# Kernel optimization log

Measured on AMD Instinct MI355X. Metric: run time of the kernel, lower is better.

The kernel has to match this reference:

```python
import jax, jax.numpy as jnp
import numpy as np

D_MODEL = 768
NUM_HEADS = 12
D_K = D_MODEL // NUM_HEADS
D_FF = 2048
LN_EPS = 1e-3  # Keras LayerNormalization default
B, S = 4, 2048


def layer_norm(x, gamma, beta):
    mu = jnp.mean(x, axis=-1, keepdims=True)
    var = jnp.var(x, axis=-1, keepdims=True)
    return (x - mu) * jax.lax.rsqrt(var + LN_EPS) * gamma + beta


def setup_inputs() -> dict:
    key = jax.random.key(0)
    ks = jax.random.split(key, 16)
    sd = 0.02
    inp = {
        "x": jax.random.normal(ks[0], (B, S, D_MODEL), dtype=jnp.float32),
        "src_mask": jnp.zeros((B, 1, 1, S), dtype=jnp.float32),
        "Wq": jax.random.normal(ks[1], (D_MODEL, D_MODEL), jnp.float32) * sd,
        "bq": jnp.zeros((D_MODEL,), jnp.float32),
        "Wk": jax.random.normal(ks[2], (D_MODEL, D_MODEL), jnp.float32) * sd,
        "bk": jnp.zeros((D_MODEL,), jnp.float32),
        "Wv": jax.random.normal(ks[3], (D_MODEL, D_MODEL), jnp.float32) * sd,
        "bv": jnp.zeros((D_MODEL,), jnp.float32),
        "Wo": jax.random.normal(ks[4], (D_MODEL, D_MODEL), jnp.float32) * sd,
        "bo": jnp.zeros((D_MODEL,), jnp.float32),
        "W1": jax.random.normal(ks[5], (D_MODEL, D_FF), jnp.float32) * sd,
        "b1": jnp.zeros((D_FF,), jnp.float32),
        "W2": jax.random.normal(ks[6], (D_FF, D_MODEL), jnp.float32) * sd,
        "b2": jnp.zeros((D_MODEL,), jnp.float32),
        "gamma1": jnp.ones((D_MODEL,), jnp.float32),
        "beta1": jnp.zeros((D_MODEL,), jnp.float32),
        "gamma2": jnp.ones((D_MODEL,), jnp.float32),
        "beta2": jnp.zeros((D_MODEL,), jnp.float32),
    }
    return inp


def encoder_layer(x, src_mask, Wq, bq, Wk, bk, Wv, bv, Wo, bo, W1, b1, W2, b2,
                  gamma1, beta1, gamma2, beta2):
    b, s, _ = x.shape
    def heads(t):  # [B,S,D] -> [B,H,S,Dk]
        return t.reshape(b, s, NUM_HEADS, D_K).transpose(0, 2, 1, 3)
    Q = heads(x @ Wq + bq)
    K = heads(x @ Wk + bk)
    V = heads(x @ Wv + bv)
    scores = jnp.einsum("bhqd,bhkd->bhqk", Q, K) / jnp.sqrt(jnp.float32(D_K))
    scores = scores + src_mask * (-1e9)
    probs = jax.nn.softmax(scores, axis=-1)
    attn = jnp.einsum("bhqk,bhkd->bhqd", probs, V)
    attn = attn.transpose(0, 2, 1, 3).reshape(b, s, D_MODEL)
    attn_out = attn @ Wo + bo
    # dropout is identity at inference
    x1 = layer_norm(x + attn_out, gamma1, beta1)
    ff = jax.nn.relu(x1 @ W1 + b1) @ W2 + b2
    return layer_norm(x1 + ff, gamma2, beta2)


def reference(x, src_mask, Wq, bq, Wk, bk, Wv, bv, Wo, bo, W1, b1, W2, b2,
              gamma1, beta1, gamma2, beta2):
    return encoder_layer(x, src_mask, Wq, bq, Wk, bk, Wv, bv, Wo, bo,
                         W1, b1, W2, b2, gamma1, beta1, gamma2, beta2)
```

## Files before the change

kernel.cpp:

```cpp
#include <hip/hip_runtime.h>


typedef unsigned short u16;
typedef __bf16 bf16x8 __attribute__((ext_vector_type(8)));
typedef __bf16 bf16x4 __attribute__((ext_vector_type(4)));
typedef unsigned short u16x8 __attribute__((ext_vector_type(8)));
typedef float f32x4 __attribute__((ext_vector_type(4)));

#define D_MODEL 768
#define D_FF    2048
#define NH      12
#define DK      64
#define S_LEN   2048
#define M_TOK   8192

#define QSCALE   0.18033688011112042f
#define MSCALE  -1.4426950408889634e9f

__device__ __forceinline__ float bf2f(u16 v) {
    union { unsigned u; float f; } c; c.u = ((unsigned)v) << 16; return c.f;
}
__device__ __forceinline__ void st_bf(u16* p, float v) { *(__bf16*)p = (__bf16)v; }

__device__ __forceinline__ void gload_lds16(const void* g, void* l) {
    __builtin_amdgcn_global_load_lds(
        (const __attribute__((address_space(1))) void*)g,
        (__attribute__((address_space(3))) void*)l, 16, 0, 0);
}

__global__ __launch_bounds__(256)
void prep_k(const float* __restrict__ x, const float* __restrict__ Wq,
            const float* __restrict__ Wk, const float* __restrict__ Wv,
            const float* __restrict__ Wo, const float* __restrict__ W1,
            const float* __restrict__ W2, u16* __restrict__ xb,
            u16* __restrict__ WqkvT, u16* __restrict__ WoT,
            u16* __restrict__ W1T, u16* __restrict__ W2T) {
    __shared__ float t[32][33];
    const int id = blockIdx.x, tid = threadIdx.x;
    if (id >= 5376) {
        const int i = ((id - 5376) * 256 + tid) * 4;
        const float4 v = *(const float4*)(x + i);
        __bf16 o[4] = {(__bf16)v.x, (__bf16)v.y, (__bf16)v.z, (__bf16)v.w};
        *(bf16x4*)(xb + i) = *(bf16x4*)o;
        return;
    }
    const float* in; u16* out; int R, C, bx, by;
    if (id < 2304) {
        const int z = id / 576, r = id % 576;
        in = z == 0 ? Wq : (z == 1 ? Wk : (z == 2 ? Wv : Wo));
        out = z == 3 ? WoT : WqkvT + z * 768 * 768;
        R = 768; C = 768; bx = (r % 24) * 32; by = (r / 24) * 32;
    } else if (id < 3840) {
        const int r = id - 2304;
        in = W1; out = W1T; R = 768; C = 2048;
        bx = (r % 64) * 32; by = (r / 64) * 32;
    } else {
        const int r = id - 3840;
        in = W2; out = W2T; R = 2048; C = 768;
        bx = (r % 24) * 32; by = (r / 24) * 32;
    }
    const int tx = tid & 31, ty = tid >> 5;
#pragma unroll
    for (int i = 0; i < 32; i += 8)
        t[ty + i][tx] = in[(size_t)(by + ty + i) * C + bx + tx];
    __syncthreads();
#pragma unroll
    for (int i = 0; i < 32; i += 8)
        st_bf(&out[(size_t)(bx + ty + i) * R + by + tx], t[tx][ty + i]);
}

__global__ __launch_bounds__(256, 3)
void qkv_gemm_k(const u16* __restrict__ A, const u16* __restrict__ Bt,
                const float* __restrict__ bq, const float* __restrict__ bk,
                const float* __restrict__ bv, u16* __restrict__ Qb,
                u16* __restrict__ Kb, u16* __restrict__ Vt) {
    __shared__ __align__(16) u16 As[2][128 * 32];
    __shared__ __align__(16) u16 Bs[2][128 * 32];
    const int tid = threadIdx.x;
    const int lane = tid & 63, w = tid >> 6;
    const int r16 = lane & 15, qd = lane >> 4;
    const int qdx = (qd ^ ((r16 >> 1) & 3)) << 3;
    const int m0 = blockIdx.x * 128, n0 = blockIdx.y * 128;
    const int wm = (w & 1) << 6, wn = (w >> 1) << 6;
    const int K = D_MODEL;

    f32x4 acc[4][4] = {};

    const u16* aP[2]; const u16* bP[2]; int f8[2];
#pragma unroll
    for (int it = 0; it < 2; ++it) {
        const int f = it * 256 + tid;
        const int row = f >> 2;
        const int kc = ((f & 3) ^ ((f >> 3) & 3)) << 3;
        aP[it] = A  + (size_t)(m0 + row) * K + kc;
        bP[it] = Bt + (size_t)(n0 + row) * K + kc;
        f8[it] = f * 8;
    }

    for (int k0 = 0; k0 < K; k0 += 64) {
#pragma unroll
        for (int p = 0; p < 2; ++p)
#pragma unroll
            for (int it = 0; it < 2; ++it) {
                gload_lds16(aP[it] + k0 + p * 32, &As[p][f8[it]]);
                gload_lds16(bP[it] + k0 + p * 32, &Bs[p][f8[it]]);
            }
        __syncthreads();
#pragma unroll
        for (int p = 0; p < 2; ++p) {
            bf16x8 af[4], bfr[4];
#pragma unroll
            for (int i = 0; i < 4; ++i) {
                af[i]  = *(const bf16x8*)&As[p][(wm + i * 16 + r16) * 32 + qdx];
                bfr[i] = *(const bf16x8*)&Bs[p][(wn + i * 16 + r16) * 32 + qdx];
            }
#pragma unroll
            for (int i = 0; i < 4; ++i)
#pragma unroll
                for (int j = 0; j < 4; ++j)
                    acc[i][j] = __builtin_amdgcn_mfma_f32_16x16x32_bf16(af[i], bfr[j], acc[i][j], 0, 0, 0);
        }
        __syncthreads();
    }

    const int sel = n0 < 768 ? 0 : (n0 < 1536 ? 1 : 2);
    const float* bias = sel == 0 ? bq : (sel == 1 ? bk : bv);
    const float scale = sel == 0 ? QSCALE : 1.0f;
    const int nbase = n0 - sel * 768;

#pragma unroll
    for (int j = 0; j < 4; ++j) {
        const int ncol = nbase + wn + j * 16 + r16;
        const float bvv = bias[ncol];
#pragma unroll
        for (int i = 0; i < 4; ++i) {
            if (sel == 2) {
                const int h = ncol >> 6, d = ncol & 63;
                const int mb = m0 + wm + i * 16 + qd * 4;
                const int bb = mb >> 11, npb = mb & 2047;
                __bf16 pk[4];
#pragma unroll
                for (int rr = 0; rr < 4; ++rr) pk[rr] = (__bf16)(acc[i][j][rr] + bvv);
                *(bf16x4*)&Vt[(((size_t)(bb * NH + h)) * DK + d) * S_LEN + npb] = *(bf16x4*)pk;
            } else {
#pragma unroll
                for (int rr = 0; rr < 4; ++rr) {
                    const int m = m0 + wm + i * 16 + qd * 4 + rr;
                    const float v = (acc[i][j][rr] + bvv) * scale;
                    if (sel == 0) st_bf(&Qb[(size_t)m * D_MODEL + ncol], v);
                    else          st_bf(&Kb[(size_t)m * D_MODEL + ncol], v);
                }
            }
        }
    }
}

__global__ __launch_bounds__(256, 3)
void gemm_bt64_k(const u16* __restrict__ A, const u16* __restrict__ Bt,
                 const float* __restrict__ bias, u16* __restrict__ Cout,
                 int M, int N, int K, int mode) {
    __shared__ __align__(16) u16 As[2][64 * 32];
    __shared__ __align__(16) u16 Bs[2][128 * 32];
    const int tid = threadIdx.x;
    const int lane = tid & 63, w = tid >> 6;
    const int r16 = lane & 15, qd = lane >> 4;
    const int qdx = (qd ^ ((r16 >> 1) & 3)) << 3;
    const int m0 = blockIdx.x * 64, n0 = blockIdx.y * 128;
    const int wm = (w & 1) << 5, wn = (w >> 1) << 6;

    f32x4 acc[2][4] = {};

    const int arow = tid >> 2;
    const int akc = (((tid & 3) ^ ((tid >> 3) & 3)) << 3);
    const u16* aP = A + (size_t)(m0 + arow) * K + akc;
    const u16* bP[2]; int f8[2];
#pragma unroll
    for (int it = 0; it < 2; ++it) {
        const int f = it * 256 + tid;
        const int row = f >> 2;
        const int kc = ((f & 3) ^ ((f >> 3) & 3)) << 3;
        bP[it] = Bt + (size_t)(n0 + row) * K + kc;
        f8[it] = f * 8;
    }

    for (int k0 = 0; k0 < K; k0 += 64) {
#pragma unroll
        for (int p = 0; p < 2; ++p) {
            gload_lds16(aP + k0 + p * 32, &As[p][tid * 8]);
#pragma unroll
            for (int it = 0; it < 2; ++it)
                gload_lds16(bP[it] + k0 + p * 32, &Bs[p][f8[it]]);
        }
        __syncthreads();
#pragma unroll
        for (int p = 0; p < 2; ++p) {
            bf16x8 af[2], bfr[4];
#pragma unroll
            for (int i = 0; i < 2; ++i)
                af[i] = *(const bf16x8*)&As[p][(wm + i * 16 + r16) * 32 + qdx];
#pragma unroll
            for (int j = 0; j < 4; ++j)
                bfr[j] = *(const bf16x8*)&Bs[p][(wn + j * 16 + r16) * 32 + qdx];
#pragma unroll
            for (int i = 0; i < 2; ++i)
#pragma unroll
                for (int j = 0; j < 4; ++j)
                    acc[i][j] = __builtin_amdgcn_mfma_f32_16x16x32_bf16(af[i], bfr[j], acc[i][j], 0, 0, 0);
        }
        __syncthreads();
    }

#pragma unroll
    for (int j = 0; j < 4; ++j) {
        const int n = n0 + wn + j * 16 + r16;
        const float bv = bias ? bias[n] : 0.0f;
#pragma unroll
        for (int i = 0; i < 2; ++i) {
#pragma unroll
            for (int rr = 0; rr < 4; ++rr) {
                const int m = m0 + wm + i * 16 + qd * 4 + rr;
                float v = acc[i][j][rr] + bv;
                if (mode == 2) v = fmaxf(v, 0.0f);
                st_bf(&Cout[(size_t)m * N + n], v);
            }
        }
    }
}

__global__ __launch_bounds__(512, 2)
void ff1_k(const u16* __restrict__ A, const u16* __restrict__ Bt,
           const float* __restrict__ bias, u16* __restrict__ C) {
    __shared__ __align__(16) u16 AB[2][32768];
    const int tid = threadIdx.x, lane = tid & 63;
    const int w = tid >> 6;
    const int wm2 = w >> 2, wn4 = w & 3;
    const int r16 = lane & 15, qd = lane >> 4;
    const int qdx = (qd ^ ((r16 >> 1) & 3)) << 3;
    const int m0 = blockIdx.x * 256, n0 = blockIdx.y * 256;
    const int K = D_MODEL, NT = 12;

    const u16* aS[4]; const u16* bS[4];
#pragma unroll
    for (int l = 0; l < 4; ++l) {
        const int f = l * 512 + tid;
        const int row = (f >> 2) & 255, ks = f >> 10;
        const int e = (((f & 3) ^ ((f >> 3) & 3)) << 3);
        aS[l] = A  + (size_t)(m0 + row) * K + ks * 32 + e;
        bS[l] = Bt + (size_t)(n0 + row) * K + ks * 32 + e;
    }

#pragma unroll
    for (int l = 0; l < 4; ++l) {
        gload_lds16(aS[l], &AB[0][(l * 512 + tid) * 8]);
        gload_lds16(bS[l], &AB[0][16384 + (l * 512 + tid) * 8]);
    }
    asm volatile("s_waitcnt vmcnt(0)" ::: "memory");
    __builtin_amdgcn_s_barrier();

    f32x4 acc[8][4] = {};
    bf16x8 af[4][2], bfr[4][2];
    const int arow0 = wm2 * 128 + r16;
    const int brow0 = wn4 * 64 + r16;

    for (int t = 0; t < NT; ++t) {
        const int cur = t & 1, nxt = cur ^ 1;
        const u16* ab = AB[cur];
        const int ka = (t + 1) * 64;
        const bool more = (t + 1) < NT;

#pragma unroll
        for (int mt = 0; mt < 4; ++mt)
#pragma unroll
            for (int ks = 0; ks < 2; ++ks)
                af[mt][ks] = *(const bf16x8*)&ab[ks * 8192 + (arow0 + mt * 16) * 32 + qdx];
#pragma unroll
        for (int nt = 0; nt < 2; ++nt)
#pragma unroll
            for (int ks = 0; ks < 2; ++ks)
                bfr[nt][ks] = *(const bf16x8*)&ab[16384 + ks * 8192 + (brow0 + nt * 16) * 32 + qdx];
        if (more) {
#pragma unroll
            for (int l = 0; l < 4; ++l)
                gload_lds16(aS[l] + ka, &AB[nxt][(l * 512 + tid) * 8]);
        }
        __builtin_amdgcn_s_setprio(1);
#pragma unroll
        for (int mt = 0; mt < 4; ++mt)
#pragma unroll
            for (int nt = 0; nt < 2; ++nt)
#pragma unroll
                for (int ks = 0; ks < 2; ++ks)
                    acc[mt][nt] = __builtin_amdgcn_mfma_f32_16x16x32_bf16(bfr[nt][ks], af[mt][ks], acc[mt][nt], 0, 0, 0);
        __builtin_amdgcn_s_setprio(0);
        __builtin_amdgcn_s_barrier();

#pragma unroll
        for (int nt = 2; nt < 4; ++nt)
#pragma unroll
            for (int ks = 0; ks < 2; ++ks)
                bfr[nt][ks] = *(const bf16x8*)&ab[16384 + ks * 8192 + (brow0 + nt * 16) * 32 + qdx];
        if (more) {
#pragma unroll
            for (int l = 0; l < 4; ++l)
                gload_lds16(bS[l] + ka, &AB[nxt][16384 + (l * 512 + tid) * 8]);
        }
        __builtin_amdgcn_s_setprio(1);
#pragma unroll
        for (int mt = 0; mt < 4; ++mt)
#pragma unroll
            for (int nt = 2; nt < 4; ++nt)
#pragma unroll
                for (int ks = 0; ks < 2; ++ks)
                    acc[mt][nt] = __builtin_amdgcn_mfma_f32_16x16x32_bf16(bfr[nt][ks], af[mt][ks], acc[mt][nt], 0, 0, 0);
        __builtin_amdgcn_s_setprio(0);
        __builtin_amdgcn_s_barrier();

#pragma unroll
        for (int mt = 0; mt < 4; ++mt)
#pragma unroll
            for (int ks = 0; ks < 2; ++ks)
                af[mt][ks] = *(const bf16x8*)&ab[ks * 8192 + (arow0 + 64 + mt * 16) * 32 + qdx];
        __builtin_amdgcn_s_setprio(1);
#pragma unroll
        for (int mt = 0; mt < 4; ++mt)
#pragma unroll
            for (int nt = 0; nt < 2; ++nt)
#pragma unroll
                for (int ks = 0; ks < 2; ++ks)
                    acc[4 + mt][nt] = __builtin_amdgcn_mfma_f32_16x16x32_bf16(bfr[nt][ks], af[mt][ks], acc[4 + mt][nt], 0, 0, 0);
        __builtin_amdgcn_s_setprio(0);
        __builtin_amdgcn_s_barrier();

        __builtin_amdgcn_s_setprio(1);
#pragma unroll
        for (int mt = 0; mt < 4; ++mt)
#pragma unroll
            for (int nt = 2; nt < 4; ++nt)
#pragma unroll
                for (int ks = 0; ks < 2; ++ks)
                    acc[4 + mt][nt] = __builtin_amdgcn_mfma_f32_16x16x32_bf16(bfr[nt][ks], af[mt][ks], acc[4 + mt][nt], 0, 0, 0);
        __builtin_amdgcn_s_setprio(0);

        if (more) {
            asm volatile("s_waitcnt vmcnt(0)" ::: "memory");
            __builtin_amdgcn_s_barrier();
        }
    }

#pragma unroll
    for (int nt = 0; nt < 4; ++nt) {
        const int nb = n0 + wn4 * 64 + nt * 16 + qd * 4;
        const float4 bv = *(const float4*)&bias[nb];
        const float b4[4] = {bv.x, bv.y, bv.z, bv.w};
#pragma unroll
        for (int mi = 0; mi < 8; ++mi) {
            const int m = m0 + wm2 * 128 + (mi >> 2) * 64 + (mi & 3) * 16 + r16;
            __bf16 pk[4];
#pragma unroll
            for (int rr = 0; rr < 4; ++rr)
                pk[rr] = (__bf16)fmaxf(acc[mi][nt][rr] + b4[rr], 0.0f);
            *(bf16x4*)&C[(size_t)m * D_FF + nb] = *(bf16x4*)pk;
        }
    }
}

#define TS 72

__global__ __launch_bounds__(256, 3)
void attn_k(const u16* __restrict__ Qg, const u16* __restrict__ Kg,
            const u16* __restrict__ Vtg, const float* __restrict__ maskg,
            u16* __restrict__ Og) {
    const int tid = threadIdx.x, lane = tid & 63, w = tid >> 6;
    const int qh = w & 1, kh = w >> 1;
    const int r16 = lane & 15, qd = lane >> 4;
    const int q0 = blockIdx.x * 128;
    const int h = blockIdx.y, b = blockIdx.z;

    __shared__ __align__(16) u16 sm[(64 + 64 + 128) * TS];
    u16* Ks  = sm;
    u16* Vts = sm + 64 * TS;
    u16* Ps  = sm + 128 * TS;

    bf16x8 qa[4][2];
#pragma unroll
    for (int mt = 0; mt < 4; ++mt)
#pragma unroll
        for (int ks = 0; ks < 2; ++ks)
            qa[mt][ks] = *(const bf16x8*)(Qg +
                ((size_t)((b * S_LEN + q0 + qh * 64 + mt * 16 + r16) * NH + h)) * DK +
                ks * 32 + qd * 8);

    const int srow = tid >> 3, sc = (tid & 7) << 3;
    const u16* vsrc = Vtg + (((size_t)(b * NH + h)) * DK) * S_LEN;
    u16x8 kreg[2], vreg[2];
#pragma unroll
    for (int it = 0; it < 2; ++it) {
        const int row = srow + it * 32;
        kreg[it] = *(const u16x8*)(Kg + ((size_t)((b * S_LEN + row) * NH + h)) * DK + sc);
        vreg[it] = *(const u16x8*)(vsrc + (size_t)row * S_LEN + sc);
    }

    float l_i[4] = {0.0f, 0.0f, 0.0f, 0.0f};
    f32x4 Oacc[4][4] = {};

    for (int kt = 0; kt < S_LEN / 64; ++kt) {
        const int ks0 = kt * 64;

#pragma unroll
        for (int it = 0; it < 2; ++it) {
            const int row = srow + it * 32;
            *(u16x8*)&Ks[row * TS + sc]  = kreg[it];
            *(u16x8*)&Vts[row * TS + sc] = vreg[it];
        }

        float4 mrow[2];
#pragma unroll
        for (int nt = 0; nt < 2; ++nt) {
            const float4 mm = ((const float4*)(maskg + (size_t)b * S_LEN + ks0))[kh * 8 + nt * 4 + qd];
            mrow[nt].x = mm.x * MSCALE; mrow[nt].y = mm.y * MSCALE;
            mrow[nt].z = mm.z * MSCALE; mrow[nt].w = mm.w * MSCALE;
        }
        __syncthreads();

        f32x4 sa[4][2];
#pragma unroll
        for (int mt = 0; mt < 4; ++mt)
#pragma unroll
            for (int nt = 0; nt < 2; ++nt) {
                sa[mt][nt][0] = mrow[nt].x; sa[mt][nt][1] = mrow[nt].y;
                sa[mt][nt][2] = mrow[nt].z; sa[mt][nt][3] = mrow[nt].w;
            }
#pragma unroll
        for (int ks = 0; ks < 2; ++ks) {
            bf16x8 kb[2];
#pragma unroll
            for (int nt = 0; nt < 2; ++nt)
                kb[nt] = *(const bf16x8*)&Ks[(kh * 32 + nt * 16 + r16) * TS + ks * 32 + qd * 8];
            __builtin_amdgcn_s_setprio(1);
#pragma unroll
            for (int mt = 0; mt < 4; ++mt)
#pragma unroll
                for (int nt = 0; nt < 2; ++nt)
                    sa[mt][nt] = __builtin_amdgcn_mfma_f32_16x16x32_bf16(kb[nt], qa[mt][ks], sa[mt][nt], 0, 0, 0);
            __builtin_amdgcn_s_setprio(0);
        }

#pragma unroll
        for (int mt = 0; mt < 4; ++mt) {
            float rsum = 0.0f;
#pragma unroll
            for (int nt = 0; nt < 2; ++nt) {
                sa[mt][nt][0] = __builtin_amdgcn_exp2f(sa[mt][nt][0]);
                sa[mt][nt][1] = __builtin_amdgcn_exp2f(sa[mt][nt][1]);
                sa[mt][nt][2] = __builtin_amdgcn_exp2f(sa[mt][nt][2]);
                sa[mt][nt][3] = __builtin_amdgcn_exp2f(sa[mt][nt][3]);
                rsum += sa[mt][nt][0] + sa[mt][nt][1] + sa[mt][nt][2] + sa[mt][nt][3];
            }
            rsum += __shfl_xor(rsum, 16);
            rsum += __shfl_xor(rsum, 32);
            l_i[mt] += rsum;
        }

#pragma unroll
        for (int mt = 0; mt < 4; ++mt)
#pragma unroll
            for (int nt = 0; nt < 2; ++nt) {
                __bf16 pk[4];
#pragma unroll
                for (int rr = 0; rr < 4; ++rr) pk[rr] = (__bf16)sa[mt][nt][rr];
                *(bf16x4*)&Ps[(qh * 64 + mt * 16 + r16) * TS + kh * 32 + nt * 16 + qd * 4] = *(bf16x4*)pk;
            }

        if (kt + 1 < S_LEN / 64) {
            const int ns0 = ks0 + 64;
#pragma unroll
            for (int it = 0; it < 2; ++it) {
                const int row = srow + it * 32;
                kreg[it] = *(const u16x8*)(Kg + ((size_t)((b * S_LEN + ns0 + row) * NH + h)) * DK + sc);
                vreg[it] = *(const u16x8*)(vsrc + (size_t)row * S_LEN + ns0 + sc);
            }
        }

        {
            bf16x8 pa[4], vb[4];
#pragma unroll
            for (int mt = 0; mt < 4; ++mt)
                pa[mt] = *(const bf16x8*)&Ps[(qh * 64 + mt * 16 + r16) * TS + kh * 32 + qd * 8];
#pragma unroll
            for (int vt = 0; vt < 4; ++vt)
                vb[vt] = *(const bf16x8*)&Vts[(vt * 16 + r16) * TS + kh * 32 + qd * 8];
            __builtin_amdgcn_s_setprio(1);
#pragma unroll
            for (int mt = 0; mt < 4; ++mt)
#pragma unroll
                for (int vt = 0; vt < 4; ++vt)
                    Oacc[mt][vt] = __builtin_amdgcn_mfma_f32_16x16x32_bf16(pa[mt], vb[vt], Oacc[mt][vt], 0, 0, 0);
            __builtin_amdgcn_s_setprio(0);
        }
        __syncthreads();
    }

    __syncthreads();
    float* mb  = (float*)sm;
    float* lsm = mb + 128 * 64;
    if (kh == 0) {
#pragma unroll
        for (int mt = 0; mt < 4; ++mt) {
            if (qd == 0) lsm[(qh * 4 + mt) * 16 + r16] = l_i[mt];
#pragma unroll
            for (int vt = 0; vt < 4; ++vt)
#pragma unroll
                for (int rr = 0; rr < 4; ++rr)
                    mb[(qh * 64 + mt * 16 + qd * 4 + rr) * 64 + vt * 16 + r16] = Oacc[mt][vt][rr];
        }
    }
    __syncthreads();
    if (kh == 1) {
#pragma unroll
        for (int mt = 0; mt < 4; ++mt) {
            const float linv = 1.0f / (l_i[mt] + lsm[(qh * 4 + mt) * 16 + r16]);
#pragma unroll
            for (int rr = 0; rr < 4; ++rr) {
                const float lr = __shfl(linv, qd * 4 + rr);
                const int qrow = q0 + qh * 64 + mt * 16 + qd * 4 + rr;
#pragma unroll
                for (int vt = 0; vt < 4; ++vt) {
                    const float o = Oacc[mt][vt][rr] +
                        mb[(qh * 64 + mt * 16 + qd * 4 + rr) * 64 + vt * 16 + r16];
                    st_bf(&Og[((size_t)((b * S_LEN + qrow) * NH + h)) * DK + vt * 16 + r16],
                          o * lr);
                }
            }
        }
    }
}

__global__ __launch_bounds__(256, 4)
void resln_k(const u16* __restrict__ xb, const u16* __restrict__ yb,
             const float* __restrict__ gamma, const float* __restrict__ beta,
             u16* __restrict__ outb, float* __restrict__ outf) {
    const int row = blockIdx.x, tid = threadIdx.x;
    const int lane = tid & 63, w = tid >> 6;
    __shared__ float redS[4], redS2[4];
    const size_t base = (size_t)row * D_MODEL;
    float h[3], s = 0.0f, s2 = 0.0f;
#pragma unroll
    for (int i = 0; i < 3; ++i) {
        const int c = i * 256 + tid;
        const float v = bf2f(xb[base + c]) + bf2f(yb[base + c]);
        h[i] = v; s += v; s2 += v * v;
    }
#pragma unroll
    for (int off = 32; off >= 1; off >>= 1) { s += __shfl_xor(s, off); s2 += __shfl_xor(s2, off); }
    if (lane == 0) { redS[w] = s; redS2[w] = s2; }
    __syncthreads();
    s  = redS[0] + redS[1] + redS[2] + redS[3];
    s2 = redS2[0] + redS2[1] + redS2[2] + redS2[3];
    const float mu  = s * (1.0f / D_MODEL);
    const float var = s2 * (1.0f / D_MODEL) - mu * mu;
    const float rstd = rsqrtf(var + 1e-3f);
#pragma unroll
    for (int i = 0; i < 3; ++i) {
        const int c = i * 256 + tid;
        const float o = (h[i] - mu) * rstd * gamma[c] + beta[c];
        if (outb) st_bf(&outb[base + c], o);
        if (outf) outf[base + c] = o;
    }
}

extern "C" void kernel_launch(void* const* d_in, const int* in_sizes, int n_in,
                              void* d_out, int out_size, void* d_ws, size_t ws_size,
                              hipStream_t stream) {
    (void)in_sizes; (void)n_in; (void)out_size; (void)ws_size;
    const float* x    = (const float*)d_in[0];
    const float* mask = (const float*)d_in[1];
    const float* Wq = (const float*)d_in[2];  const float* bq  = (const float*)d_in[3];
    const float* Wk = (const float*)d_in[4];  const float* bk  = (const float*)d_in[5];
    const float* Wv = (const float*)d_in[6];  const float* bv  = (const float*)d_in[7];
    const float* Wo = (const float*)d_in[8];  const float* bo  = (const float*)d_in[9];
    const float* W1 = (const float*)d_in[10]; const float* b1  = (const float*)d_in[11];
    const float* W2 = (const float*)d_in[12]; const float* b2  = (const float*)d_in[13];
    const float* g1 = (const float*)d_in[14]; const float* be1 = (const float*)d_in[15];
    const float* g2 = (const float*)d_in[16]; const float* be2 = (const float*)d_in[17];

    char* ws = (char*)d_ws;
    u16* xb     = (u16*)(ws + 0);
    u16* WqkvT  = (u16*)(ws + 12582912);
    u16* WoT    = (u16*)(ws + 16121856);
    u16* W1T    = (u16*)(ws + 17301504);
    u16* W2T    = (u16*)(ws + 20447232);
    u16* Qb     = (u16*)(ws + 23592960);
    u16* Kb     = (u16*)(ws + 36175872);
    u16* Vtg    = (u16*)(ws + 48758784);
    u16* Ab     = (u16*)(ws + 61341696);
    u16* Yb     = (u16*)(ws + 73924608);
    u16* X1b    = (u16*)(ws + 86507520);
    u16* H1b    = (u16*)(ws + 23592960);
    u16* Y2b    = (u16*)(ws + 73924608);

    const dim3 blk(256);

    prep_k<<<dim3(11520), blk, 0, stream>>>(x, Wq, Wk, Wv, Wo, W1, W2,
                                            xb, WqkvT, WoT, W1T, W2T);

    qkv_gemm_k<<<dim3(64, 18), blk, 0, stream>>>(xb, WqkvT, bq, bk, bv, Qb, Kb, Vtg);

    attn_k<<<dim3(16, NH, 4), blk, 0, stream>>>(Qb, Kb, Vtg, mask, Ab);

    gemm_bt64_k<<<dim3(128, 6), blk, 0, stream>>>(Ab, WoT, bo, Yb, M_TOK, D_MODEL, D_MODEL, 1);

    resln_k<<<dim3(M_TOK), blk, 0, stream>>>(xb, Yb, g1, be1, X1b, nullptr);

    ff1_k<<<dim3(32, 8), dim3(512), 0, stream>>>(X1b, W1T, b1, H1b);

    gemm_bt64_k<<<dim3(128, 6), blk, 0, stream>>>(H1b, W2T, b2, Y2b, M_TOK, D_MODEL, D_FF, 1);

    resln_k<<<dim3(M_TOK), blk, 0, stream>>>(X1b, Y2b, g2, be2, nullptr, (float*)d_out);
}
```

Measured before the change: 340.6 us.

## Replace output-projection and FF2 GEMM with 128x128 double-buffered pipelined kernel

Swaps the 64x128 tile GEMM used for the Wo projection and the second FFN matmul for a 128x128 tile kernel. The new kernel double-buffers LDS, issues the next tile's global loads between the two halves of MFMA work, and raises wave priority during MFMA. Operands are swapped so each lane holds four consecutive N columns, allowing vectorised bf16x4 stores and float4 bias loads. This gives more reuse per tile and overlaps loads with compute. The cost is fewer blocks (384) on a large-CU GPU, which may underfill the device, plus higher register use.

```diff
diff --git a/kernel.cpp b/kernel.cpp
--- a/kernel.cpp
+++ b/kernel.cpp
@@ -155,74 +155,113 @@
     }
 }
 
-__global__ __launch_bounds__(256, 3)
-void gemm_bt64_k(const u16* __restrict__ A, const u16* __restrict__ Bt,
-                 const float* __restrict__ bias, u16* __restrict__ Cout,
-                 int M, int N, int K, int mode) {
-    __shared__ __align__(16) u16 As[2][64 * 32];
-    __shared__ __align__(16) u16 Bs[2][128 * 32];
-    const int tid = threadIdx.x;
-    const int lane = tid & 63, w = tid >> 6;
+__global__ __launch_bounds__(256, 2)
+void g4p_k(const u16* __restrict__ A, const u16* __restrict__ Bt,
+           const float* __restrict__ bias, u16* __restrict__ Cout,
+           int N, int K) {
+    __shared__ __align__(16) u16 AB[2][16384];
+    const int tid = threadIdx.x, lane = tid & 63;
+    const int w = tid >> 6;
+    const int wm2 = w >> 1, wn2 = w & 1;
     const int r16 = lane & 15, qd = lane >> 4;
     const int qdx = (qd ^ ((r16 >> 1) & 3)) << 3;
-    const int m0 = blockIdx.x * 64, n0 = blockIdx.y * 128;
-    const int wm = (w & 1) << 5, wn = (w >> 1) << 6;
-
-    f32x4 acc[2][4] = {};
-
-    const int arow = tid >> 2;
-    const int akc = (((tid & 3) ^ ((tid >> 3) & 3)) << 3);
-    const u16* aP = A + (size_t)(m0 + arow) * K + akc;
-    const u16* bP[2]; int f8[2];
-#pragma unroll
-    for (int it = 0; it < 2; ++it) {
-        const int f = it * 256 + tid;
-        const int row = f >> 2;
-        const int kc = ((f & 3) ^ ((f >> 3) & 3)) << 3;
-        bP[it] = Bt + (size_t)(n0 + row) * K + kc;
-        f8[it] = f * 8;
-    }
-
-    for (int k0 = 0; k0 < K; k0 += 64) {
-#pragma unroll
-        for (int p = 0; p < 2; ++p) {
-            gload_lds16(aP + k0 + p * 32, &As[p][tid * 8]);
-#pragma unroll
-            for (int it = 0; it < 2; ++it)
-                gload_lds16(bP[it] + k0 + p * 32, &Bs[p][f8[it]]);
-        }
-        __syncthreads();
-#pragma unroll
-        for (int p = 0; p < 2; ++p) {
-            bf16x8 af[2], bfr[4];
-#pragma unroll
-            for (int i = 0; i < 2; ++i)
-                af[i] = *(const bf16x8*)&As[p][(wm + i * 16 + r16) * 32 + qdx];
-#pragma unroll
-            for (int j = 0; j < 4; ++j)
-                bfr[j] = *(const bf16x8*)&Bs[p][(wn + j * 16 + r16) * 32 + qdx];
-#pragma unroll
-            for (int i = 0; i < 2; ++i)
-#pragma unroll
-                for (int j = 0; j < 4; ++j)
-                    acc[i][j] = __builtin_amdgcn_mfma_f32_16x16x32_bf16(af[i], bfr[j], acc[i][j], 0, 0, 0);
-        }
-        __syncthreads();
-    }
-
-#pragma unroll
-    for (int j = 0; j < 4; ++j) {
-        const int n = n0 + wn + j * 16 + r16;
-        const float bv = bias ? bias[n] : 0.0f;
-#pragma unroll
-        for (int i = 0; i < 2; ++i) {
-#pragma unroll
-            for (int rr = 0; rr < 4; ++rr) {
-                const int m = m0 + wm + i * 16 + qd * 4 + rr;
-                float v = acc[i][j][rr] + bv;
-                if (mode == 2) v = fmaxf(v, 0.0f);
-                st_bf(&Cout[(size_t)m * N + n], v);
-            }
+    const int m0 = blockIdx.x * 128, n0 = blockIdx.y * 128;
+    const int NT = K >> 6;
+
+    const u16* aS[4]; const u16* bS[4];
+#pragma unroll
+    for (int l = 0; l < 4; ++l) {
+        const int f = l * 256 + tid;
+        const int row = (f >> 2) & 127, ks = f >> 9;
+        const int e = (((f & 3) ^ ((f >> 3) & 3)) << 3);
+        aS[l] = A  + (size_t)(m0 + row) * K + ks * 32 + e;
+        bS[l] = Bt + (size_t)(n0 + row) * K + ks * 32 + e;
+    }
+
+#pragma unroll
+    for (int l = 0; l < 4; ++l) {
+        gload_lds16(aS[l], &AB[0][(l * 256 + tid) * 8]);
+        gload_lds16(bS[l], &AB[0][8192 + (l * 256 + tid) * 8]);
+    }
+    asm volatile("s_waitcnt vmcnt(0)" ::: "memory");
+    __builtin_amdgcn_s_barrier();
+
+    f32x4 acc[4][4] = {};
+    bf16x8 af[4][2], bfr[4][2];
+    const int arow0 = wm2 * 64 + r16;
+    const int brow0 = wn2 * 64 + r16;
+
+    for (int t = 0; t < NT; ++t) {
+        const int cur = t & 1, nxt = cur ^ 1;
+        const u16* ab = AB[cur];
+        const int ka = (t + 1) * 64;
+        const bool more = (t + 1) < NT;
+
+#pragma unroll
+        for (int mt = 0; mt < 4; ++mt)
+#pragma unroll
+            for (int ks = 0; ks < 2; ++ks)
+                af[mt][ks] = *(const bf16x8*)&ab[ks * 4096 + (arow0 + mt * 16) * 32 + qdx];
+#pragma unroll
+        for (int nt = 0; nt < 2; ++nt)
+#pragma unroll
+            for (int ks = 0; ks < 2; ++ks)
+                bfr[nt][ks] = *(const bf16x8*)&ab[8192 + ks * 4096 + (brow0 + nt * 16) * 32 + qdx];
+        if (more) {
+#pragma unroll
+            for (int l = 0; l < 4; ++l)
+                gload_lds16(aS[l] + ka, &AB[nxt][(l * 256 + tid) * 8]);
+        }
+        __builtin_amdgcn_s_setprio(1);
+#pragma unroll
+        for (int mt = 0; mt < 4; ++mt)
+#pragma unroll
+            for (int nt = 0; nt < 2; ++nt)
+#pragma unroll
+                for (int ks = 0; ks < 2; ++ks)
+                    acc[mt][nt] = __builtin_amdgcn_mfma_f32_16x16x32_bf16(bfr[nt][ks], af[mt][ks], acc[mt][nt], 0, 0, 0);
+        __builtin_amdgcn_s_setprio(0);
+        __builtin_amdgcn_s_barrier();
+
+#pragma unroll
+        for (int nt = 2; nt < 4; ++nt)
+#pragma unroll
+            for (int ks = 0; ks < 2; ++ks)
+                bfr[nt][ks] = *(const bf16x8*)&ab[8192 + ks * 4096 + (brow0 + nt * 16) * 32 + qdx];
+        if (more) {
+#pragma unroll
+            for (int l = 0; l < 4; ++l)
+                gload_lds16(bS[l] + ka, &AB[nxt][8192 + (l * 256 + tid) * 8]);
+        }
+        __builtin_amdgcn_s_setprio(1);
+#pragma unroll
+        for (int mt = 0; mt < 4; ++mt)
+#pragma unroll
+            for (int nt = 2; nt < 4; ++nt)
+#pragma unroll
+                for (int ks = 0; ks < 2; ++ks)
+                    acc[mt][nt] = __builtin_amdgcn_mfma_f32_16x16x32_bf16(bfr[nt][ks], af[mt][ks], acc[mt][nt], 0, 0, 0);
+        __builtin_amdgcn_s_setprio(0);
+
+        if (more) {
+            asm volatile("s_waitcnt vmcnt(0)" ::: "memory");
+            __builtin_amdgcn_s_barrier();
+        }
+    }
+
+#pragma unroll
+    for (int nt = 0; nt < 4; ++nt) {
+        const int nb = n0 + wn2 * 64 + nt * 16 + qd * 4;
+        const float4 bv = *(const float4*)&bias[nb];
+        const float b4[4] = {bv.x, bv.y, bv.z, bv.w};
+#pragma unroll
+        for (int mi = 0; mi < 4; ++mi) {
+            const int m = m0 + wm2 * 64 + mi * 16 + r16;
+            __bf16 pk[4];
+#pragma unroll
+            for (int rr = 0; rr < 4; ++rr)
+                pk[rr] = (__bf16)(acc[mi][nt][rr] + b4[rr]);
+            *(bf16x4*)&Cout[(size_t)m * N + nb] = *(bf16x4*)pk;
         }
     }
 }
@@ -607,13 +646,13 @@
 
     attn_k<<<dim3(16, NH, 4), blk, 0, stream>>>(Qb, Kb, Vtg, mask, Ab);
 
-    gemm_bt64_k<<<dim3(128, 6), blk, 0, stream>>>(Ab, WoT, bo, Yb, M_TOK, D_MODEL, D_MODEL, 1);
+    g4p_k<<<dim3(64, 6), blk, 0, stream>>>(Ab, WoT, bo, Yb, D_MODEL, D_MODEL);
 
     resln_k<<<dim3(M_TOK), blk, 0, stream>>>(xb, Yb, g1, be1, X1b, nullptr);
 
     ff1_k<<<dim3(32, 8), dim3(512), 0, stream>>>(X1b, W1T, b1, H1b);
 
-    gemm_bt64_k<<<dim3(128, 6), blk, 0, stream>>>(H1b, W2T, b2, Y2b, M_TOK, D_MODEL, D_FF, 1);
+    g4p_k<<<dim3(64, 6), blk, 0, stream>>>(H1b, W2T, b2, Y2b, D_MODEL, D_FF);
 
     resln_k<<<dim3(M_TOK), blk, 0, stream>>>(X1b, Y2b, g2, be2, nullptr, (float*)d_out);
 }
```

Result: faster. 330.5 us (-3.0%).
